# Performance work log

Measured on AMD Instinct MI355X. Metric: run time of the kernel, lower is better.

The kernel has to match this reference:

```python
import jax, jax.numpy as jnp
import numpy as np

B, G, I, E = 256, 24, 512, 512


def setup_inputs() -> dict:
    key = jax.random.key(0)
    k1, k2 = jax.random.split(key)
    inp = jax.random.normal(k1, (B, G, I), dtype=jnp.float32)
    weights = jax.random.normal(k2, (G, I, E), dtype=jnp.float32) * (1.0 / np.sqrt(E))
    bias = 0.1 * jnp.ones((E,), dtype=jnp.float32)
    # Cyclic group inverse-index table: row h is the permutation g -> (g - h) mod G,
    # matching symmetry_group.index2inverse_indices[h] (each row a valid permutation).
    g_ar = np.arange(G)
    inv_indices = jnp.asarray((g_ar[None, :] - g_ar[:, None]) % G, dtype=jnp.int32)
    return {"input": inp, "weights": weights, "bias": bias, "inv_indices": inv_indices}


def reference(input, weights, bias, inv_indices):
    # conv_filter[h, g, i, e] = weights[inv_indices[h, g], i, e]   -> [G, G, I, E]
    conv_filter = weights[inv_indices]
    # (input[:,None,:,:,None] * filter[None]).sum(2).sum(2) == einsum over g, i
    out = jnp.einsum("bgi,hgie->bhe", input, conv_filter)  # [B, G, E]
    return out + bias
```

## Files before the change

kernel.cpp:

```cpp
#include <hip/hip_runtime.h>
#include <hip/hip_bf16.h>
#include <stdint.h>

#define G_ 24
#define B_ 256
#define I_ 512
#define E_ 512
#define K_ (G_ * I_)
#define SPLITK 2
#define NT_SPLIT (K_ / 64 / SPLITK)

typedef __bf16 bf16x8 __attribute__((ext_vector_type(8)));
typedef float f32x4 __attribute__((ext_vector_type(4)));

__global__ void cvt_in_kernel(const float* __restrict__ in, __hip_bfloat16* __restrict__ out, int n4) {
  int idx = blockIdx.x * blockDim.x + threadIdx.x;
  if (idx >= n4) return;
  float4 v = reinterpret_cast<const float4*>(in)[idx];
  union { __hip_bfloat16 h[4]; uint2 u; } pk;
  pk.h[0] = __float2bfloat16(v.x);
  pk.h[1] = __float2bfloat16(v.y);
  pk.h[2] = __float2bfloat16(v.z);
  pk.h[3] = __float2bfloat16(v.w);
  reinterpret_cast<uint2*>(out)[idx] = pk.u;
}

__global__ void transpose_w_kernel(const float* __restrict__ W, __hip_bfloat16* __restrict__ Wt) {
  __shared__ float tile[32][33];
  const int g = blockIdx.z;
  const int i0 = blockIdx.x * 32;
  const int e0 = blockIdx.y * 32;
  const float* src = W + (size_t)g * (I_ * E_) + (size_t)(i0 + threadIdx.y) * E_ + e0 + threadIdx.x;
  #pragma unroll
  for (int r = 0; r < 32; r += 8)
    tile[threadIdx.y + r][threadIdx.x] = src[(size_t)r * E_];
  __syncthreads();
  __hip_bfloat16* dst = Wt + (size_t)g * (I_ * E_) + (size_t)(e0 + threadIdx.y) * I_ + i0 + threadIdx.x;
  #pragma unroll
  for (int r = 0; r < 32; r += 8)
    dst[(size_t)r * I_] = __float2bfloat16(tile[threadIdx.x][threadIdx.y + r]);
}

__global__ void init_out_kernel(const float* __restrict__ bias, float* __restrict__ out, int n4) {
  int idx = blockIdx.x * blockDim.x + threadIdx.x;
  if (idx >= n4) return;
  int e4 = idx & 127;
  reinterpret_cast<float4*>(out)[idx] = reinterpret_cast<const float4*>(bias)[e4];
}

__global__ __launch_bounds__(256) void gemm_kernel(
    const __hip_bfloat16* __restrict__ A,
    const __hip_bfloat16* __restrict__ Wt,
    float* __restrict__ out) {

  __shared__ __align__(16) __hip_bfloat16 ldsA[2][128 * 64];
  __shared__ __align__(16) __hip_bfloat16 ldsB[2][64 * 64];

  const int tid  = threadIdx.x;
  const int lane = tid & 63;
  const int wave = tid >> 6;
  const int h     = blockIdx.z >> 1;
  const int split = blockIdx.z & 1;
  const int m0 = blockIdx.y * 128;
  const int n0 = blockIdx.x * 64;

  const int wr = wave >> 1;
  const int wc = wave & 1;
  const int rsel = lane & 15;
  const int q    = lane >> 4;

  f32x4 acc[4][2];
  #pragma unroll
  for (int i = 0; i < 4; ++i)
    #pragma unroll
    for (int j = 0; j < 2; ++j)
      acc[i][j] = (f32x4){0.f, 0.f, 0.f, 0.f};

  auto stage = [&](int t, int buf) {
    const int g  = t >> 3;
    const int i0 = (t & 7) * 64;
    int gsrc = g - h; if (gsrc < 0) gsrc += G_;
    const __hip_bfloat16* Abase = A  + (size_t)m0 * K_ + (size_t)t * 64;
    const __hip_bfloat16* Bbase = Wt + (size_t)gsrc * (I_ * E_) + (size_t)n0 * I_ + i0;
    #pragma unroll
    for (int j = 0; j < 4; ++j) {
      int c    = j * 256 + tid;
      int row  = c >> 3;
      int slot = (c & 7) ^ (row & 7);
      const __hip_bfloat16* ga = Abase + (size_t)row * K_ + slot * 8;
      __builtin_amdgcn_global_load_lds((const __attribute__((address_space(1))) void*)ga,
          (__attribute__((address_space(3))) void*)&ldsA[buf][(size_t)c * 8], 16, 0, 0);
    }
    #pragma unroll
    for (int j = 0; j < 2; ++j) {
      int c    = j * 256 + tid;
      int row  = c >> 3;
      int slot = (c & 7) ^ (row & 7);
      const __hip_bfloat16* gb = Bbase + (size_t)row * I_ + slot * 8;
      __builtin_amdgcn_global_load_lds((const __attribute__((address_space(1))) void*)gb,
          (__attribute__((address_space(3))) void*)&ldsB[buf][(size_t)c * 8], 16, 0, 0);
    }
  };

  const int t0 = split * NT_SPLIT;
  int cur = 0;
  stage(t0, 0);

  for (int lt = 0; lt < NT_SPLIT; ++lt) {
    const int t = t0 + lt;
    if (lt + 1 < NT_SPLIT) {
      stage(t + 1, cur ^ 1);
      asm volatile("s_waitcnt vmcnt(6)" ::: "memory");
    } else {
      asm volatile("s_waitcnt vmcnt(0)" ::: "memory");
    }
    __builtin_amdgcn_s_barrier();
    asm volatile("" ::: "memory");

    const __hip_bfloat16* Al = &ldsA[cur][0];
    const __hip_bfloat16* Bl = &ldsB[cur][0];
    #pragma unroll
    for (int kk = 0; kk < 2; ++kk) {
      const int kslot = kk * 4 + q;
      bf16x8 af[4], bfr[2];
      #pragma unroll
      for (int mi = 0; mi < 4; ++mi) {
        int r = wr * 64 + mi * 16 + rsel;
        int lin = kslot ^ (r & 7);
        af[mi] = *(const bf16x8*)(Al + (size_t)r * 64 + lin * 8);
      }
      #pragma unroll
      for (int ni = 0; ni < 2; ++ni) {
        int r = wc * 32 + ni * 16 + rsel;
        int lin = kslot ^ (r & 7);
        bfr[ni] = *(const bf16x8*)(Bl + (size_t)r * 64 + lin * 8);
      }
      #pragma unroll
      for (int mi = 0; mi < 4; ++mi)
        #pragma unroll
        for (int ni = 0; ni < 2; ++ni)
          acc[mi][ni] = __builtin_amdgcn_mfma_f32_16x16x32_bf16(af[mi], bfr[ni], acc[mi][ni], 0, 0, 0);
    }

    asm volatile("s_waitcnt lgkmcnt(0)" ::: "memory");
    __builtin_amdgcn_s_barrier();
    asm volatile("" ::: "memory");
    cur ^= 1;
  }

  #pragma unroll
  for (int mi = 0; mi < 4; ++mi) {
    #pragma unroll
    for (int ni = 0; ni < 2; ++ni) {
      int col  = n0 + wc * 32 + ni * 16 + (lane & 15);
      int rowb = m0 + wr * 64 + mi * 16 + (lane >> 4) * 4;
      float* o = out + (size_t)rowb * (G_ * E_) + (size_t)h * E_ + col;
      #pragma unroll
      for (int r = 0; r < 4; ++r)
        atomicAdd(o + (size_t)r * (G_ * E_), acc[mi][ni][r]);
    }
  }
}

extern "C" void kernel_launch(void* const* d_in, const int* in_sizes, int n_in,
                              void* d_out, int out_size, void* d_ws, size_t ws_size,
                              hipStream_t stream) {
  const float* in   = (const float*)d_in[0];
  const float* w    = (const float*)d_in[1];
  const float* bias = (const float*)d_in[2];
  float* out = (float*)d_out;

  __hip_bfloat16* A_bf = (__hip_bfloat16*)d_ws;
  __hip_bfloat16* Wt   = (__hip_bfloat16*)((char*)d_ws + (size_t)B_ * K_ * 2);

  const int n4in  = (B_ * K_) / 4;
  const int n4out = (B_ * G_ * E_) / 4;
  cvt_in_kernel<<<n4in / 256, 256, 0, stream>>>(in, A_bf, n4in);
  transpose_w_kernel<<<dim3(E_ / 32, I_ / 32, G_), dim3(32, 8), 0, stream>>>(w, Wt);
  init_out_kernel<<<n4out / 256, 256, 0, stream>>>(bias, out, n4out);
  gemm_kernel<<<dim3(E_ / 64, B_ / 128, G_ * SPLITK), 256, 0, stream>>>(A_bf, Wt, out);
}
```

Measured before the change: 123.4 us.

## Use 256x256 GEMM tiles with 512 threads, split-K 5 and ping-pong pipeline

Replaces the 128x64 tile GEMM with a 256x256 tile kernel on 512 threads. The whole batch is covered by one M tile, and split-K rises from 2 to 5 with uneven split lengths. Each K tile is split into four sub-phases that interleave half-tile global-to-LDS loads with MFMA, using setprio and explicit vmcnt waits. The goal is more operand reuse per LDS byte and better overlap of loads and compute. The cost is heavy register and LDS pressure (64KB LDS), fewer blocks, and more atomic traffic from the extra splits.

```diff
diff --git a/kernel.cpp b/kernel.cpp
--- a/kernel.cpp
+++ b/kernel.cpp
@@ -7,17 +7,17 @@
 #define I_ 512
 #define E_ 512
 #define K_ (G_ * I_)
-#define SPLITK 2
-#define NT_SPLIT (K_ / 64 / SPLITK)
-
+#define SPLITK 5
+
+typedef __hip_bfloat16 bf16;
 typedef __bf16 bf16x8 __attribute__((ext_vector_type(8)));
 typedef float f32x4 __attribute__((ext_vector_type(4)));
 
-__global__ void cvt_in_kernel(const float* __restrict__ in, __hip_bfloat16* __restrict__ out, int n4) {
+__global__ void cvt_in_kernel(const float* __restrict__ in, bf16* __restrict__ out, int n4) {
   int idx = blockIdx.x * blockDim.x + threadIdx.x;
   if (idx >= n4) return;
   float4 v = reinterpret_cast<const float4*>(in)[idx];
-  union { __hip_bfloat16 h[4]; uint2 u; } pk;
+  union { bf16 h[4]; uint2 u; } pk;
   pk.h[0] = __float2bfloat16(v.x);
   pk.h[1] = __float2bfloat16(v.y);
   pk.h[2] = __float2bfloat16(v.z);
@@ -25,7 +25,7 @@
   reinterpret_cast<uint2*>(out)[idx] = pk.u;
 }
 
-__global__ void transpose_w_kernel(const float* __restrict__ W, __hip_bfloat16* __restrict__ Wt) {
+__global__ void transpose_w_kernel(const float* __restrict__ W, bf16* __restrict__ Wt) {
   __shared__ float tile[32][33];
   const int g = blockIdx.z;
   const int i0 = blockIdx.x * 32;
@@ -35,7 +35,7 @@
   for (int r = 0; r < 32; r += 8)
     tile[threadIdx.y + r][threadIdx.x] = src[(size_t)r * E_];
   __syncthreads();
-  __hip_bfloat16* dst = Wt + (size_t)g * (I_ * E_) + (size_t)(e0 + threadIdx.y) * I_ + i0 + threadIdx.x;
+  bf16* dst = Wt + (size_t)g * (I_ * E_) + (size_t)(e0 + threadIdx.y) * I_ + i0 + threadIdx.x;
   #pragma unroll
   for (int r = 0; r < 32; r += 8)
     dst[(size_t)r * I_] = __float2bfloat16(tile[threadIdx.x][threadIdx.y + r]);
@@ -48,113 +48,156 @@
   reinterpret_cast<float4*>(out)[idx] = reinterpret_cast<const float4*>(bias)[e4];
 }
 
-__global__ __launch_bounds__(256) void gemm_kernel(
-    const __hip_bfloat16* __restrict__ A,
-    const __hip_bfloat16* __restrict__ Wt,
+
+#define FENCE() asm volatile("" ::: "memory")
+#define BAR()   __builtin_amdgcn_s_barrier()
+#define LGKM0() do { asm volatile("s_waitcnt lgkmcnt(0)" ::: "memory"); \
+                     __builtin_amdgcn_sched_barrier(0); } while (0)
+#define VMW(N)  asm volatile("s_waitcnt vmcnt(" #N ")" ::: "memory")
+
+__device__ __forceinline__ void gload16(const bf16* g, bf16* l) {
+  __builtin_amdgcn_global_load_lds((const __attribute__((address_space(1))) void*)g,
+                                   (__attribute__((address_space(3))) void*)l, 16, 0, 0);
+}
+
+__global__ __launch_bounds__(512, 2) void gemm256_kernel(
+    const bf16* __restrict__ A,
+    const bf16* __restrict__ Wt,
     float* __restrict__ out) {
 
-  __shared__ __align__(16) __hip_bfloat16 ldsA[2][128 * 64];
-  __shared__ __align__(16) __hip_bfloat16 ldsB[2][64 * 64];
+  __shared__ __align__(16) bf16 lds[2][2][256 * 64];
 
   const int tid  = threadIdx.x;
   const int lane = tid & 63;
   const int wave = tid >> 6;
-  const int h     = blockIdx.z >> 1;
-  const int split = blockIdx.z & 1;
-  const int m0 = blockIdx.y * 128;
-  const int n0 = blockIdx.x * 64;
-
-  const int wr = wave >> 1;
-  const int wc = wave & 1;
+  const int wr   = wave >> 2;
+  const int wc   = wave & 3;
   const int rsel = lane & 15;
   const int q    = lane >> 4;
 
-  f32x4 acc[4][2];
-  #pragma unroll
-  for (int i = 0; i < 4; ++i)
-    #pragma unroll
-    for (int j = 0; j < 2; ++j)
+  const int h     = blockIdx.z / SPLITK;
+  const int split = blockIdx.z % SPLITK;
+  const int n0    = blockIdx.x * 256;
+
+  const int T0 = split * 38 + (split < 2 ? split : 2);
+  const int NT = 38 + (split < 2 ? 1 : 0);
+
+  f32x4 acc[8][4];
+  #pragma unroll
+  for (int i = 0; i < 8; ++i)
+    #pragma unroll
+    for (int j = 0; j < 4; ++j)
       acc[i][j] = (f32x4){0.f, 0.f, 0.f, 0.f};
 
-  auto stage = [&](int t, int buf) {
-    const int g  = t >> 3;
-    const int i0 = (t & 7) * 64;
+  auto stageA = [&](int t, int half, int b) {
+    const bf16* Ab = A + (size_t)t * 64;
+    #pragma unroll
+    for (int j = 0; j < 2; ++j) {
+      int quarter = half + j * 2;
+      int row  = quarter * 64 + (tid >> 3);
+      int slot = (tid & 7) ^ ((tid >> 3) & 7);
+      gload16(Ab + (size_t)row * K_ + slot * 8,
+              &lds[b][0][(size_t)(quarter * 512 + tid) * 8]);
+    }
+  };
+  auto stageB = [&](int t, int half, int b) {
+    int g = t >> 3, i0 = (t & 7) * 64;
     int gsrc = g - h; if (gsrc < 0) gsrc += G_;
-    const __hip_bfloat16* Abase = A  + (size_t)m0 * K_ + (size_t)t * 64;
-    const __hip_bfloat16* Bbase = Wt + (size_t)gsrc * (I_ * E_) + (size_t)n0 * I_ + i0;
-    #pragma unroll
-    for (int j = 0; j < 4; ++j) {
-      int c    = j * 256 + tid;
-      int row  = c >> 3;
-      int slot = (c & 7) ^ (row & 7);
-      const __hip_bfloat16* ga = Abase + (size_t)row * K_ + slot * 8;
-      __builtin_amdgcn_global_load_lds((const __attribute__((address_space(1))) void*)ga,
-          (__attribute__((address_space(3))) void*)&ldsA[buf][(size_t)c * 8], 16, 0, 0);
-    }
+    const bf16* Wb = Wt + (size_t)gsrc * (I_ * E_) + (size_t)n0 * I_ + i0;
     #pragma unroll
     for (int j = 0; j < 2; ++j) {
-      int c    = j * 256 + tid;
-      int row  = c >> 3;
-      int slot = (c & 7) ^ (row & 7);
-      const __hip_bfloat16* gb = Bbase + (size_t)row * I_ + slot * 8;
-      __builtin_amdgcn_global_load_lds((const __attribute__((address_space(1))) void*)gb,
-          (__attribute__((address_space(3))) void*)&ldsB[buf][(size_t)c * 8], 16, 0, 0);
-    }
-  };
-
-  const int t0 = split * NT_SPLIT;
-  int cur = 0;
-  stage(t0, 0);
-
-  for (int lt = 0; lt < NT_SPLIT; ++lt) {
-    const int t = t0 + lt;
-    if (lt + 1 < NT_SPLIT) {
-      stage(t + 1, cur ^ 1);
-      asm volatile("s_waitcnt vmcnt(6)" ::: "memory");
-    } else {
-      asm volatile("s_waitcnt vmcnt(0)" ::: "memory");
-    }
-    __builtin_amdgcn_s_barrier();
-    asm volatile("" ::: "memory");
-
-    const __hip_bfloat16* Al = &ldsA[cur][0];
-    const __hip_bfloat16* Bl = &ldsB[cur][0];
-    #pragma unroll
-    for (int kk = 0; kk < 2; ++kk) {
-      const int kslot = kk * 4 + q;
-      bf16x8 af[4], bfr[2];
-      #pragma unroll
-      for (int mi = 0; mi < 4; ++mi) {
-        int r = wr * 64 + mi * 16 + rsel;
-        int lin = kslot ^ (r & 7);
-        af[mi] = *(const bf16x8*)(Al + (size_t)r * 64 + lin * 8);
-      }
-      #pragma unroll
-      for (int ni = 0; ni < 2; ++ni) {
-        int r = wc * 32 + ni * 16 + rsel;
-        int lin = kslot ^ (r & 7);
-        bfr[ni] = *(const bf16x8*)(Bl + (size_t)r * 64 + lin * 8);
-      }
+      int u    = j * 512 + tid;
+      int band = u >> 8;
+      int rowb = band * 64 + half * 32 + ((u >> 3) & 31);
+      int slot = (u & 7) ^ ((u >> 3) & 7);
+      gload16(Wb + (size_t)rowb * I_ + slot * 8,
+              &lds[b][1][(size_t)(rowb * 8 + (u & 7)) * 8]);
+    }
+  };
+
+  bf16x8 af[8];
+  bf16x8 b0f[4];
+  bf16x8 b1f[4];
+  auto readA = [&](int mhalf, int b, bf16x8* dst) {
+    const bf16* p = &lds[b][0][0];
+    #pragma unroll
+    for (int mi = 0; mi < 4; ++mi) {
+      int r   = wr * 128 + (mhalf * 4 + mi) * 16 + rsel;
+      int off = r * 64 + (q ^ (r & 7)) * 8;
+      dst[mi * 2 + 0] = *(const bf16x8*)(p + off);
+      dst[mi * 2 + 1] = *(const bf16x8*)(p + (off ^ 32));
+    }
+  };
+  auto readB = [&](int nhalf, int b, bf16x8* dst) {
+    const bf16* p = &lds[b][1][0];
+    #pragma unroll
+    for (int ni = 0; ni < 2; ++ni) {
+      int r   = wc * 64 + (nhalf * 2 + ni) * 16 + rsel;
+      int off = r * 64 + (q ^ (r & 7)) * 8;
+      dst[ni * 2 + 0] = *(const bf16x8*)(p + off);
+      dst[ni * 2 + 1] = *(const bf16x8*)(p + (off ^ 32));
+    }
+  };
+  auto MMA = [&](int miB, int niB, bf16x8* a, bf16x8* bb) {
+    #pragma unroll
+    for (int kk = 0; kk < 2; ++kk)
       #pragma unroll
       for (int mi = 0; mi < 4; ++mi)
         #pragma unroll
         for (int ni = 0; ni < 2; ++ni)
-          acc[mi][ni] = __builtin_amdgcn_mfma_f32_16x16x32_bf16(af[mi], bfr[ni], acc[mi][ni], 0, 0, 0);
-    }
-
-    asm volatile("s_waitcnt lgkmcnt(0)" ::: "memory");
-    __builtin_amdgcn_s_barrier();
-    asm volatile("" ::: "memory");
-    cur ^= 1;
+          acc[miB + mi][niB + ni] = __builtin_amdgcn_mfma_f32_16x16x32_bf16(
+              a[mi * 2 + kk], bb[ni * 2 + kk], acc[miB + mi][niB + ni], 0, 0, 0);
+  };
+
+#define KTILE(T, S1A, S1B, S2A, S2B, VMPH0, VMPH3) do {                         \
+                                           \
+    if (S1A) stageA((T) + 1, 1, buf ^ 1);                                       \
+    readA(0, buf, af); readB(0, buf, b0f);                                      \
+    FENCE(); BAR(); LGKM0();                                                    \
+    __builtin_amdgcn_s_setprio(1); MMA(0, 0, af, b0f); __builtin_amdgcn_s_setprio(0); \
+    VMPH0; FENCE(); BAR();                                                      \
+                                                    \
+    if (S1B) stageB((T) + 1, 1, buf ^ 1);                                       \
+    readB(1, buf, b1f);                                                         \
+    FENCE(); BAR(); LGKM0();                                                    \
+    __builtin_amdgcn_s_setprio(1); MMA(0, 2, af, b1f); __builtin_amdgcn_s_setprio(0); \
+    FENCE(); BAR();                                                             \
+                                                    \
+    if (S2A) stageA((T) + 2, 0, buf);                                           \
+    readA(1, buf, af);                                                          \
+    FENCE(); BAR(); LGKM0();                                                    \
+    __builtin_amdgcn_s_setprio(1); MMA(4, 2, af, b1f); __builtin_amdgcn_s_setprio(0); \
+    FENCE(); BAR();                                                             \
+                                                    \
+    if (S2B) stageB((T) + 2, 0, buf);                                           \
+    FENCE(); BAR();                                                             \
+    __builtin_amdgcn_s_setprio(1); MMA(4, 0, af, b0f); __builtin_amdgcn_s_setprio(0); \
+    VMPH3; FENCE(); BAR();                                                      \
+    buf ^= 1;                                                                   \
+  } while (0)
+
+  stageA(T0, 0, 0); stageB(T0, 0, 0);
+  stageA(T0, 1, 0); stageB(T0, 1, 0);
+  stageA(T0 + 1, 0, 1); stageB(T0 + 1, 0, 1);
+  VMW(8);
+  FENCE(); BAR();
+
+  int buf = 0;
+  for (int lt = 0; lt + 2 < NT; ++lt) {
+    KTILE(T0 + lt, true, true, true, true, VMW(6), VMW(8));
   }
-
-  #pragma unroll
-  for (int mi = 0; mi < 4; ++mi) {
-    #pragma unroll
-    for (int ni = 0; ni < 2; ++ni) {
-      int col  = n0 + wc * 32 + ni * 16 + (lane & 15);
-      int rowb = m0 + wr * 64 + mi * 16 + (lane >> 4) * 4;
-      float* o = out + (size_t)rowb * (G_ * E_) + (size_t)h * E_ + col;
+  KTILE(T0 + NT - 2, true, true, false, false, VMW(6), VMW(4));
+  KTILE(T0 + NT - 1, false, false, false, false, VMW(0), ((void)0));
+
+#undef KTILE
+
+  #pragma unroll
+  for (int mi = 0; mi < 8; ++mi) {
+    #pragma unroll
+    for (int ni = 0; ni < 4; ++ni) {
+      int ecol  = n0 + wc * 64 + ni * 16 + (lane & 15);
+      int brow0 = wr * 128 + mi * 16 + (lane >> 4) * 4;
+      float* o = out + (size_t)brow0 * (G_ * E_) + (size_t)h * E_ + ecol;
       #pragma unroll
       for (int r = 0; r < 4; ++r)
         atomicAdd(o + (size_t)r * (G_ * E_), acc[mi][ni][r]);
@@ -170,13 +213,13 @@
   const float* bias = (const float*)d_in[2];
   float* out = (float*)d_out;
 
-  __hip_bfloat16* A_bf = (__hip_bfloat16*)d_ws;
-  __hip_bfloat16* Wt   = (__hip_bfloat16*)((char*)d_ws + (size_t)B_ * K_ * 2);
+  bf16* A_bf = (bf16*)d_ws;
+  bf16* Wt   = (bf16*)((char*)d_ws + (size_t)B_ * K_ * 2);
 
   const int n4in  = (B_ * K_) / 4;
   const int n4out = (B_ * G_ * E_) / 4;
   cvt_in_kernel<<<n4in / 256, 256, 0, stream>>>(in, A_bf, n4in);
   transpose_w_kernel<<<dim3(E_ / 32, I_ / 32, G_), dim3(32, 8), 0, stream>>>(w, Wt);
   init_out_kernel<<<n4out / 256, 256, 0, stream>>>(bias, out, n4out);
-  gemm_kernel<<<dim3(E_ / 64, B_ / 128, G_ * SPLITK), 256, 0, stream>>>(A_bf, Wt, out);
-}
+  gemm256_kernel<<<dim3(E_ / 256, 1, G_ * SPLITK), 512, 0, stream>>>(A_bf, Wt, out);
+}
```

Result: slower. 132.5 us (+7.3%).

## Enlarge GEMM tile to 128x128, split-K by four, swizzle block order

Applied to the files above, without the earlier changes.

The GEMM block tile grows from 128x64 to 128x128, so each wave computes a 64x64 sub-tile with a 4x4 MFMA accumulator set and fetches fewer operand bytes per FLOP. Split-K goes from 2 to 4, which keeps the grid at 768 blocks. The 3D grid becomes a flat 1D grid with a swizzled block-to-tile mapping meant to improve L2 locality. Launch bounds request 2 blocks per CU. The cost is twice as many atomic adds into the output, higher register pressure, and 64 KB of LDS per block.

```diff
diff --git a/kernel.cpp b/kernel.cpp
--- a/kernel.cpp
+++ b/kernel.cpp
@@ -7,17 +7,18 @@
 #define I_ 512
 #define E_ 512
 #define K_ (G_ * I_)
-#define SPLITK 2
-#define NT_SPLIT (K_ / 64 / SPLITK)
+#define SPLITK 4
+#define NTILES 48
 
+typedef __hip_bfloat16 bf16;
 typedef __bf16 bf16x8 __attribute__((ext_vector_type(8)));
 typedef float f32x4 __attribute__((ext_vector_type(4)));
 
-__global__ void cvt_in_kernel(const float* __restrict__ in, __hip_bfloat16* __restrict__ out, int n4) {
+__global__ void cvt_in_kernel(const float* __restrict__ in, bf16* __restrict__ out, int n4) {
   int idx = blockIdx.x * blockDim.x + threadIdx.x;
   if (idx >= n4) return;
   float4 v = reinterpret_cast<const float4*>(in)[idx];
-  union { __hip_bfloat16 h[4]; uint2 u; } pk;
+  union { bf16 h[4]; uint2 u; } pk;
   pk.h[0] = __float2bfloat16(v.x);
   pk.h[1] = __float2bfloat16(v.y);
   pk.h[2] = __float2bfloat16(v.z);
@@ -25,7 +26,7 @@
   reinterpret_cast<uint2*>(out)[idx] = pk.u;
 }
 
-__global__ void transpose_w_kernel(const float* __restrict__ W, __hip_bfloat16* __restrict__ Wt) {
+__global__ void transpose_w_kernel(const float* __restrict__ W, bf16* __restrict__ Wt) {
   __shared__ float tile[32][33];
   const int g = blockIdx.z;
   const int i0 = blockIdx.x * 32;
@@ -35,7 +36,7 @@
   for (int r = 0; r < 32; r += 8)
     tile[threadIdx.y + r][threadIdx.x] = src[(size_t)r * E_];
   __syncthreads();
-  __hip_bfloat16* dst = Wt + (size_t)g * (I_ * E_) + (size_t)(e0 + threadIdx.y) * I_ + i0 + threadIdx.x;
+  bf16* dst = Wt + (size_t)g * (I_ * E_) + (size_t)(e0 + threadIdx.y) * I_ + i0 + threadIdx.x;
   #pragma unroll
   for (int r = 0; r < 32; r += 8)
     dst[(size_t)r * I_] = __float2bfloat16(tile[threadIdx.x][threadIdx.y + r]);
@@ -48,113 +49,110 @@
   reinterpret_cast<float4*>(out)[idx] = reinterpret_cast<const float4*>(bias)[e4];
 }
 
-__global__ __launch_bounds__(256) void gemm_kernel(
-    const __hip_bfloat16* __restrict__ A,
-    const __hip_bfloat16* __restrict__ Wt,
+__global__ __launch_bounds__(256, 2) void gemm_kernel(
+    const bf16* __restrict__ A,
+    const bf16* __restrict__ Wt,
     float* __restrict__ out) {
 
-  __shared__ __align__(16) __hip_bfloat16 ldsA[2][128 * 64];
-  __shared__ __align__(16) __hip_bfloat16 ldsB[2][64 * 64];
+  __shared__ __align__(16) bf16 lds[2][2][128 * 64];
 
   const int tid  = threadIdx.x;
   const int lane = tid & 63;
   const int wave = tid >> 6;
-  const int h     = blockIdx.z >> 1;
-  const int split = blockIdx.z & 1;
-  const int m0 = blockIdx.y * 128;
-  const int n0 = blockIdx.x * 64;
-
-  const int wr = wave >> 1;
-  const int wc = wave & 1;
+  const int wr   = wave >> 1;
+  const int wc   = wave & 1;
   const int rsel = lane & 15;
   const int q    = lane >> 4;
 
-  f32x4 acc[4][2];
+  const int bid = blockIdx.x;
+  const int swz = (bid & 7) * 96 + (bid >> 3);
+  const int n0 = (swz & 3) * 128;
+  const int m0 = ((swz >> 2) & 1) * 128;
+  const int hs = swz >> 3;
+  const int h  = hs >> 2;
+  const int T0 = (hs & 3) * NTILES;
+
+  f32x4 acc[4][4];
   #pragma unroll
   for (int i = 0; i < 4; ++i)
     #pragma unroll
-    for (int j = 0; j < 2; ++j)
+    for (int j = 0; j < 4; ++j)
       acc[i][j] = (f32x4){0.f, 0.f, 0.f, 0.f};
 
   auto stage = [&](int t, int buf) {
     const int g  = t >> 3;
     const int i0 = (t & 7) * 64;
     int gsrc = g - h; if (gsrc < 0) gsrc += G_;
-    const __hip_bfloat16* Abase = A  + (size_t)m0 * K_ + (size_t)t * 64;
-    const __hip_bfloat16* Bbase = Wt + (size_t)gsrc * (I_ * E_) + (size_t)n0 * I_ + i0;
+    const bf16* Abase = A  + (size_t)m0 * K_ + (size_t)t * 64;
+    const bf16* Bbase = Wt + (size_t)gsrc * (I_ * E_) + (size_t)n0 * I_ + i0;
     #pragma unroll
     for (int j = 0; j < 4; ++j) {
       int c    = j * 256 + tid;
       int row  = c >> 3;
       int slot = (c & 7) ^ (row & 7);
-      const __hip_bfloat16* ga = Abase + (size_t)row * K_ + slot * 8;
-      __builtin_amdgcn_global_load_lds((const __attribute__((address_space(1))) void*)ga,
-          (__attribute__((address_space(3))) void*)&ldsA[buf][(size_t)c * 8], 16, 0, 0);
+      __builtin_amdgcn_global_load_lds(
+          (const __attribute__((address_space(1))) void*)(Abase + (size_t)row * K_ + slot * 8),
+          (__attribute__((address_space(3))) void*)&lds[buf][0][(size_t)c * 8], 16, 0, 0);
     }
     #pragma unroll
-    for (int j = 0; j < 2; ++j) {
+    for (int j = 0; j < 4; ++j) {
       int c    = j * 256 + tid;
       int row  = c >> 3;
       int slot = (c & 7) ^ (row & 7);
-      const __hip_bfloat16* gb = Bbase + (size_t)row * I_ + slot * 8;
-      __builtin_amdgcn_global_load_lds((const __attribute__((address_space(1))) void*)gb,
-          (__attribute__((address_space(3))) void*)&ldsB[buf][(size_t)c * 8], 16, 0, 0);
+      __builtin_amdgcn_global_load_lds(
+          (const __attribute__((address_space(1))) void*)(Bbase + (size_t)row * I_ + slot * 8),
+          (__attribute__((address_space(3))) void*)&lds[buf][1][(size_t)c * 8], 16, 0, 0);
     }
   };
 
-  const int t0 = split * NT_SPLIT;
-  int cur = 0;
-  stage(t0, 0);
+  stage(T0, 0);
 
-  for (int lt = 0; lt < NT_SPLIT; ++lt) {
-    const int t = t0 + lt;
-    if (lt + 1 < NT_SPLIT) {
-      stage(t + 1, cur ^ 1);
-      asm volatile("s_waitcnt vmcnt(6)" ::: "memory");
+  for (int lt = 0; lt < NTILES; ++lt) {
+    const int cur = lt & 1;
+    if (lt + 1 < NTILES) {
+      stage(T0 + lt + 1, cur ^ 1);
+      asm volatile("s_waitcnt vmcnt(8)" ::: "memory");
     } else {
       asm volatile("s_waitcnt vmcnt(0)" ::: "memory");
     }
     __builtin_amdgcn_s_barrier();
     asm volatile("" ::: "memory");
 
-    const __hip_bfloat16* Al = &ldsA[cur][0];
-    const __hip_bfloat16* Bl = &ldsB[cur][0];
+    const bf16* Al = &lds[cur][0][0];
+    const bf16* Bl = &lds[cur][1][0];
     #pragma unroll
     for (int kk = 0; kk < 2; ++kk) {
       const int kslot = kk * 4 + q;
-      bf16x8 af[4], bfr[2];
+      bf16x8 af[4], bfr[4];
       #pragma unroll
       for (int mi = 0; mi < 4; ++mi) {
         int r = wr * 64 + mi * 16 + rsel;
-        int lin = kslot ^ (r & 7);
-        af[mi] = *(const bf16x8*)(Al + (size_t)r * 64 + lin * 8);
+        af[mi] = *(const bf16x8*)(Al + (size_t)r * 64 + (kslot ^ (r & 7)) * 8);
       }
       #pragma unroll
-      for (int ni = 0; ni < 2; ++ni) {
-        int r = wc * 32 + ni * 16 + rsel;
-        int lin = kslot ^ (r & 7);
-        bfr[ni] = *(const bf16x8*)(Bl + (size_t)r * 64 + lin * 8);
+      for (int ni = 0; ni < 4; ++ni) {
+        int r = wc * 64 + ni * 16 + rsel;
+        bfr[ni] = *(const bf16x8*)(Bl + (size_t)r * 64 + (kslot ^ (r & 7)) * 8);
       }
       #pragma unroll
       for (int mi = 0; mi < 4; ++mi)
         #pragma unroll
-        for (int ni = 0; ni < 2; ++ni)
+        for (int ni = 0; ni < 4; ++ni)
           acc[mi][ni] = __builtin_amdgcn_mfma_f32_16x16x32_bf16(af[mi], bfr[ni], acc[mi][ni], 0, 0, 0);
     }
 
     asm volatile("s_waitcnt lgkmcnt(0)" ::: "memory");
     __builtin_amdgcn_s_barrier();
     asm volatile("" ::: "memory");
-    cur ^= 1;
   }
 
   #pragma unroll
   for (int mi = 0; mi < 4; ++mi) {
     #pragma unroll
-    for (int ni = 0; ni < 2; ++ni) {
-      int col  = n0 + wc * 32 + ni * 16 + (lane & 15);
-      int rowb = m0 + wr * 64 + mi * 16 + (lane >> 4) * 4;
-      float* o = out + (size_t)rowb * (G_ * E_) + (size_t)h * E_ + col;
+    for (int ni = 0; ni < 4; ++ni) {
+      int ecol  = n0 + wc * 64 + ni * 16 + (lane & 15);
+      int brow0 = m0 + wr * 64 + mi * 16 + (lane >> 4) * 4;
+      float* o = out + (size_t)brow0 * (G_ * E_) + (size_t)h * E_ + ecol;
       #pragma unroll
       for (int r = 0; r < 4; ++r)
         atomicAdd(o + (size_t)r * (G_ * E_), acc[mi][ni][r]);
@@ -170,13 +168,13 @@
   const float* bias = (const float*)d_in[2];
   float* out = (float*)d_out;
 
-  __hip_bfloat16* A_bf = (__hip_bfloat16*)d_ws;
-  __hip_bfloat16* Wt   = (__hip_bfloat16*)((char*)d_ws + (size_t)B_ * K_ * 2);
+  bf16* A_bf = (bf16*)d_ws;
+  bf16* Wt   = (bf16*)((char*)d_ws + (size_t)B_ * K_ * 2);
 
   const int n4in  = (B_ * K_) / 4;
   const int n4out = (B_ * G_ * E_) / 4;
   cvt_in_kernel<<<n4in / 256, 256, 0, stream>>>(in, A_bf, n4in);
   transpose_w_kernel<<<dim3(E_ / 32, I_ / 32, G_), dim3(32, 8), 0, stream>>>(w, Wt);
   init_out_kernel<<<n4out / 256, 256, 0, stream>>>(bias, out, n4out);
-  gemm_kernel<<<dim3(E_ / 64, B_ / 128, G_ * SPLITK), 256, 0, stream>>>(A_bf, Wt, out);
+  gemm_kernel<<<768, 256, 0, stream>>>(A_bf, Wt, out);
 }
```

Result: no change. 124.8 us (+1.2%).
